# Performance work log

Hardware: AMD Instinct MI355X
Metric: run time of the kernel (lower is better)

Reference implementation:

```python
import jax, jax.numpy as jnp
import numpy as np

B, N, D, HID, NB, NC = 64, 256, 1024, 512, 2, 1000
EPS = 1e-5

def _ln(x, g, b):
    m = x.mean(-1, keepdims=True)
    v = ((x - m) ** 2).mean(-1, keepdims=True)
    return (x - m) / jnp.sqrt(v + EPS) * g + b

def _gelu(x):
    return jax.nn.gelu(x, approximate=False)

def _knn_adjacency(x, k):
    # x: [N, D] -> symmetric-normalized kNN adjacency with self loops, [N, N]
    n = x.shape[0]
    sq = jnp.sum(x * x, axis=-1)
    d2 = sq[:, None] + sq[None, :] - 2.0 * (x @ x.T)
    d2 = jnp.where(jnp.eye(n, dtype=bool), jnp.inf, d2)  # exclude self from kNN
    idx = jax.lax.top_k(-d2, k)[1]                       # [N, k] nearest neighbors
    A = jnp.zeros((n, n), x.dtype).at[jnp.arange(n)[:, None], idx].set(1.0)
    A = jnp.maximum(A, A.T) + jnp.eye(n, dtype=x.dtype)  # symmetrize + self loops
    dinv = jax.lax.rsqrt(A.sum(-1))                      # D^{-1/2}
    return A * dinv[:, None] * dinv[None, :]

def setup_inputs() -> dict:
    key = jax.random.key(0)
    ks = jax.random.split(key, 8)
    s = lambda i, shape: jax.random.normal(ks[i], shape, jnp.float32) * 0.02
    return {
        "tokens": jax.random.normal(ks[0], (B, N, D), jnp.float32),
        "W1": s(1, (NB, D, HID)), "b1": jnp.zeros((NB, HID), jnp.float32),
        "W2": s(2, (NB, HID, D)), "b2": jnp.zeros((NB, D), jnp.float32),
        "g1": jnp.ones((NB, D), jnp.float32), "be1": jnp.zeros((NB, D), jnp.float32),
        "g2": jnp.ones((NB, D), jnp.float32), "be2": jnp.zeros((NB, D), jnp.float32),
        "gr": jnp.ones((D,), jnp.float32), "br": jnp.zeros((D,), jnp.float32),
        "Wc": s(3, (D, NC)), "bc": jnp.zeros((NC,), jnp.float32),
        "k": 8,
    }

def reference(tokens, W1, b1, W2, b2, g1, be1, g2, be2, gr, br, Wc, bc, k):
    # tokens: [B, N, D] backbone features flattened to nodes (eval mode: dropout = identity)
    A = jax.vmap(lambda t: _knn_adjacency(t, k))(tokens)  # [B, N, N]
    x = tokens
    for i in range(NB):  # GraphBlock
        h = _ln(x, g1[i], be1[i])
        h = _gelu(jnp.einsum("bij,bjh->bih", A, h @ W1[i] + b1[i]))  # A_hat @ lin1
        h = jnp.einsum("bij,bjd->bid", A, h @ W2[i] + b2[i])          # A_hat @ lin2
        x = x + h
        x = x + _gelu(_ln(x, g2[i], be2[i]))
    x = _gelu(_ln(x, gr, br))      # readout
    out = x.mean(axis=1)           # graph mean-pool, [B, D]
    return out @ Wc + bc           # logits [B, NC]
```

## Files before the change

### kernel.cpp

```cpp
#include <hip/hip_runtime.h>
#include <hip/hip_bf16.h>
#include <math.h>

constexpr int Bb  = 64;
constexpr int Nn_ = 256;
constexpr int Dd  = 1024;
constexpr int Hh  = 512;
constexpr int NC  = 1000;
constexpr float LN_EPS = 1e-5f;

#define DEV __device__ __forceinline__

typedef unsigned short u16;
typedef __attribute__((ext_vector_type(8))) short bf16x8;
typedef __attribute__((ext_vector_type(4))) float f32x4;
typedef __attribute__((ext_vector_type(4))) unsigned short u16x4;

DEV float erf_fast(float x) {
    const float ax = fabsf(x);
    const float t = __builtin_amdgcn_rcpf(fmaf(0.3275911f, ax, 1.0f));
    const float y = t * (0.254829592f + t * (-0.284496736f + t * (1.421413741f +
                    t * (-1.453152027f + t * 1.061405429f))));
    const float r = 1.0f - y * __expf(-ax * ax);
    return copysignf(r, x);
}
DEV float gelu_f(float x) { return 0.5f * x * (1.0f + erf_fast(x * 0.70710678118654752f)); }
DEV u16 bfb(float x) { __hip_bfloat16 h = __float2bfloat16(x); u16 u; __builtin_memcpy(&u, &h, 2); return u; }
DEV float fromb(u16 u) { unsigned int w = (unsigned int)u << 16; float f; __builtin_memcpy(&f, &w, 4); return f; }

DEV void gload16(const void* g, void* l) {
    __builtin_amdgcn_global_load_lds(
        (const __attribute__((address_space(1))) void*)(uintptr_t)g,
        (__attribute__((address_space(3))) void*)(uintptr_t)l, 16, 0, 0);
}

enum { EP_SBIAS_BF = 3 };

template<int EPI>
__global__ __launch_bounds__(512) void mgemm_k(
    const u16* __restrict__ Ag, const u16* __restrict__ Bg, void* __restrict__ Cg,
    const float* __restrict__ bias, const float* __restrict__ rsA,
    int M, int Nc, int K, long sA, long sB, long sC,
    int lognx, int logny, int lognz)
{
    __shared__ __align__(16) u16 sm[2][2][128 * 32];
    const int tid = threadIdx.x;
    const int l = tid & 63, w = tid >> 6;
    const int wm = w >> 2, wn = w & 3;

    const int lid = blockIdx.x;
    const int xcd = lid & 7, idx = lid >> 3;
    int bxi, byi, z;
    if (lognz == 0) {
        bxi = idx & ((1 << lognx) - 1);
        byi = (xcd << (logny - 3)) | (idx >> lognx);
        z = 0;
    } else {
        bxi = idx & ((1 << lognx) - 1);
        byi = (idx >> lognx) & ((1 << logny) - 1);
        z = (xcd << (lognz - 3)) | (idx >> (lognx + logny));
    }
    const int bm = byi * 128, bn = bxi * 128;

    const u16* Ab  = Ag + (long)z * sA;
    const u16* Bbp = Bg + (long)z * sB;

    f32x4 acc[4][2] = {};
    const int nt = K >> 5;

    auto stage = [&](int db, int t) {
        const long kk = (long)t << 5;
        const int o = tid * 16;
        const int r = o >> 6;
        const int g = ((o >> 4) & 3) ^ ((r >> 1) & 3);
        gload16(Ab  + (long)(bm + r) * K + kk + g * 8, (char*)&sm[db][0][0] + o);
        gload16(Bbp + (long)(bn + r) * K + kk + g * 8, (char*)&sm[db][1][0] + o);
    };

    stage(0, 0);
    __syncthreads();
    for (int t = 0; t < nt; ++t) {
        const int db = t & 1;
        if (t + 1 < nt) stage(db ^ 1, t + 1);
        const int lr = l & 15, g = l >> 4;
        bf16x8 af[4], bfr[2];
        #pragma unroll
        for (int fm = 0; fm < 4; ++fm) {
            const int r = wm * 64 + fm * 16 + lr;
            af[fm] = *(const bf16x8*)((const char*)&sm[db][0][0] + r * 64 + ((g ^ ((r >> 1) & 3)) << 4));
        }
        #pragma unroll
        for (int fn = 0; fn < 2; ++fn) {
            const int r = wn * 32 + fn * 16 + lr;
            bfr[fn] = *(const bf16x8*)((const char*)&sm[db][1][0] + r * 64 + ((g ^ ((r >> 1) & 3)) << 4));
        }
        #pragma unroll
        for (int fm = 0; fm < 4; ++fm)
            #pragma unroll
            for (int fn = 0; fn < 2; ++fn)
                acc[fm][fn] = __builtin_amdgcn_mfma_f32_16x16x32_bf16(af[fm], bfr[fn], acc[fm][fn], 0, 0, 0);
        __syncthreads();
    }

    const int lr = l & 15, lg = l >> 4;
    u16* Cb = (u16*)Cg;
    #pragma unroll
    for (int fm = 0; fm < 4; ++fm)
        #pragma unroll
        for (int fn = 0; fn < 2; ++fn) {
            const int gc = bn + wn * 32 + fn * 16 + lr;
            const float bv = bias[gc];
            #pragma unroll
            for (int rg = 0; rg < 4; ++rg) {
                const int gm = bm + wm * 64 + fm * 16 + lg * 4 + rg;
                Cb[(long)gm * Nc + gc] = bfb(acc[fm][fn][rg] + rsA[gm] * bv);
            }
        }
}

__global__ __launch_bounds__(512) __attribute__((amdgpu_waves_per_eu(2, 2))) void ayy2_k(
    const u16* __restrict__ Ahat, const u16* __restrict__ LN1, const u16* __restrict__ W1t,
    const float* __restrict__ b1, u16* __restrict__ AZ)
{
    __shared__ __align__(16) char smem[131072];
    u16* sY = (u16*)smem;
    u16* sZ = (u16*)(smem + 65536);
    char* stA = smem + 65536;
    char* stB = smem + 65536 + 32768;

    const int tid = threadIdx.x;
    const int l = tid & 63, w = tid >> 6;
    const int lr = l & 15, g = l >> 4;

    const int lid = blockIdx.x;
    const int xcd = lid & 7, idx = lid >> 3;
    const int cs = idx & 3;
    const int z  = xcd * 8 + (idx >> 2);

    const u16* Ab  = Ahat + (long)z * Nn_ * Nn_;
    const u16* Lb  = LN1 + (long)z * Nn_ * Dd;
    const u16* Wsl = W1t + (long)(cs * 128) * Dd;
    const float* bsl = b1 + cs * 128;

    {
        const int rm = w >> 1, cn = w & 1;
        f32x4 acc[4][4] = {};

        auto stage0 = [&](int db, int t) {
            const long kk = (long)t << 5;
            #pragma unroll
            for (int i = 0; i < 2; ++i) {
                const int o = i * 8192 + tid * 16;
                const int r = o >> 6;
                const int gg = ((o >> 4) & 3) ^ ((r >> 1) & 3);
                gload16(Lb + (long)r * Dd + kk + gg * 8, stA + db * 16384 + o);
            }
            {
                const int o = tid * 16;
                const int c = o >> 6;
                const int gg = ((o >> 4) & 3) ^ ((c >> 1) & 3);
                gload16(Wsl + (long)c * Dd + kk + gg * 8, stB + db * 8192 + o);
            }
        };

        stage0(0, 0);
        __syncthreads();
        for (int t = 0; t < 32; ++t) {
            const int db = t & 1;
            if (t + 1 < 32) stage0(db ^ 1, t + 1);
            bf16x8 af[4], bfr[4];
            #pragma unroll
            for (int fm = 0; fm < 4; ++fm) {
                const int r = rm * 64 + fm * 16 + lr;
                af[fm] = *(const bf16x8*)(stA + db * 16384 + r * 64 + ((g ^ ((r >> 1) & 3)) << 4));
            }
            #pragma unroll
            for (int fn = 0; fn < 4; ++fn) {
                const int c = cn * 64 + fn * 16 + lr;
                bfr[fn] = *(const bf16x8*)(stB + db * 8192 + c * 64 + ((g ^ ((c >> 1) & 3)) << 4));
            }
            #pragma unroll
            for (int fm = 0; fm < 4; ++fm)
                #pragma unroll
                for (int fn = 0; fn < 4; ++fn)
                    acc[fm][fn] = __builtin_amdgcn_mfma_f32_16x16x32_bf16(af[fm], bfr[fn], acc[fm][fn], 0, 0, 0);
            __syncthreads();
        }
        #pragma unroll
        for (int fm = 0; fm < 4; ++fm)
            #pragma unroll
            for (int fn = 0; fn < 4; ++fn) {
                const int c = cn * 64 + fn * 16 + lr;
                const int n0 = rm * 64 + fm * 16 + g * 4;
                const float bv = bsl[c];
                u16x4 v;
                #pragma unroll
                for (int rg = 0; rg < 4; ++rg) v[rg] = bfb(acc[fm][fn][rg] + bv);
                *(u16x4*)((char*)sY + c * 512 + ((n0 * 2) ^ ((c & 7) << 4))) = v;
            }
    }

    const int wm = w >> 1, wn = w & 1;
    bf16x8 afh[4][8];
    #pragma unroll
    for (int fm = 0; fm < 4; ++fm) {
        const int r = wm * 64 + fm * 16 + lr;
        #pragma unroll
        for (int ks = 0; ks < 8; ++ks)
            afh[fm][ks] = *(const bf16x8*)(Ab + (long)r * Nn_ + ks * 32 + g * 8);
    }

    __syncthreads();

    f32x4 acc[4][4] = {};
    #pragma unroll
    for (int ks = 0; ks < 8; ++ks) {
        bf16x8 bfr[4];
        #pragma unroll
        for (int fn = 0; fn < 4; ++fn) {
            const int c = wn * 64 + fn * 16 + lr;
            const int kb = (ks * 64 + g * 16) ^ ((c & 7) << 4);
            bfr[fn] = *(const bf16x8*)((const char*)sY + c * 512 + kb);
        }
        #pragma unroll
        for (int fm = 0; fm < 4; ++fm)
            #pragma unroll
            for (int fn = 0; fn < 4; ++fn)
                acc[fm][fn] = __builtin_amdgcn_mfma_f32_16x16x32_bf16(afh[fm][ks], bfr[fn], acc[fm][fn], 0, 0, 0);
    }
    #pragma unroll
    for (int fm = 0; fm < 4; ++fm)
        #pragma unroll
        for (int fn = 0; fn < 4; ++fn) {
            const int c = wn * 64 + fn * 16 + lr;
            const int r0 = wm * 64 + fm * 16 + g * 4;
            u16x4 v;
            #pragma unroll
            for (int rg = 0; rg < 4; ++rg) v[rg] = bfb(gelu_f(acc[fm][fn][rg]));
            *(u16x4*)((char*)sZ + c * 512 + ((r0 * 2) ^ ((c & 7) << 4))) = v;
            acc[fm][fn] = f32x4{0.f, 0.f, 0.f, 0.f};
        }
    __syncthreads();

    #pragma unroll
    for (int ks = 0; ks < 8; ++ks) {
        bf16x8 bfr[4];
        #pragma unroll
        for (int fn = 0; fn < 4; ++fn) {
            const int c = wn * 64 + fn * 16 + lr;
            const int kb = (ks * 64 + g * 16) ^ ((c & 7) << 4);
            bfr[fn] = *(const bf16x8*)((const char*)sZ + c * 512 + kb);
        }
        #pragma unroll
        for (int fm = 0; fm < 4; ++fm)
            #pragma unroll
            for (int fn = 0; fn < 4; ++fn)
                acc[fm][fn] = __builtin_amdgcn_mfma_f32_16x16x32_bf16(afh[fm][ks], bfr[fn], acc[fm][fn], 0, 0, 0);
    }
    u16* Ob = AZ + (long)z * Nn_ * Hh + cs * 128;
    #pragma unroll
    for (int fm = 0; fm < 4; ++fm)
        #pragma unroll
        for (int fn = 0; fn < 4; ++fn)
            #pragma unroll
            for (int rg = 0; rg < 4; ++rg) {
                const int r = wm * 64 + fm * 16 + g * 4 + rg;
                const int c = wn * 64 + fn * 16 + lr;
                Ob[(long)r * Hh + c] = bfb(acc[fm][fn][rg]);
            }
}

__global__ __launch_bounds__(512) void d2mm_k(
    const u16* __restrict__ HL, const float* __restrict__ sq, float* __restrict__ d2)
{
    __shared__ __align__(16) u16 sm[2][4][128 * 32];
    const int tid = threadIdx.x;
    const int l = tid & 63, w = tid >> 6;
    const int wm = w >> 2, wn = w & 3;

    const int lid = blockIdx.x;
    const int xcd = lid & 7, q = lid >> 3;
    const int j   = q % 3;
    const int z   = (q / 3) * 8 + xcd;
    const int bm  = (j == 2) ? 128 : 0;
    const int bn  = (j == 0) ? 0 : 128;

    const u16* Hb = HL + (long)z * Nn_ * 2048;

    f32x4 acc[4][2] = {};

    auto stage = [&](int db, int t) {
        const long kk = (long)t << 5;
        const int o = tid * 16;
        const int r = o >> 6;
        const int g = ((o >> 4) & 3) ^ ((r >> 1) & 3);
        const long ka = kk + g * 8;
        gload16(Hb + (long)(bm + r) * 2048 + ka,        (char*)&sm[db][0][0] + o);
        gload16(Hb + (long)(bm + r) * 2048 + 1024 + ka, (char*)&sm[db][1][0] + o);
        gload16(Hb + (long)(bn + r) * 2048 + ka,        (char*)&sm[db][2][0] + o);
        gload16(Hb + (long)(bn + r) * 2048 + 1024 + ka, (char*)&sm[db][3][0] + o);
    };

    stage(0, 0);
    __syncthreads();
    for (int t = 0; t < 32; ++t) {
        const int db = t & 1;
        if (t + 1 < 32) stage(db ^ 1, t + 1);
        const int lr = l & 15, g = l >> 4;
        bf16x8 ah[4], al[4], bh[2], bl[2];
        #pragma unroll
        for (int fm = 0; fm < 4; ++fm) {
            const int r = wm * 64 + fm * 16 + lr;
            const int off = r * 64 + ((g ^ ((r >> 1) & 3)) << 4);
            ah[fm] = *(const bf16x8*)((const char*)&sm[db][0][0] + off);
            al[fm] = *(const bf16x8*)((const char*)&sm[db][1][0] + off);
        }
        #pragma unroll
        for (int fn = 0; fn < 2; ++fn) {
            const int r = wn * 32 + fn * 16 + lr;
            const int off = r * 64 + ((g ^ ((r >> 1) & 3)) << 4);
            bh[fn] = *(const bf16x8*)((const char*)&sm[db][2][0] + off);
            bl[fn] = *(const bf16x8*)((const char*)&sm[db][3][0] + off);
        }
        #pragma unroll
        for (int fm = 0; fm < 4; ++fm)
            #pragma unroll
            for (int fn = 0; fn < 2; ++fn) {
                acc[fm][fn] = __builtin_amdgcn_mfma_f32_16x16x32_bf16(ah[fm], bh[fn], acc[fm][fn], 0, 0, 0);
                acc[fm][fn] = __builtin_amdgcn_mfma_f32_16x16x32_bf16(ah[fm], bl[fn], acc[fm][fn], 0, 0, 0);
                acc[fm][fn] = __builtin_amdgcn_mfma_f32_16x16x32_bf16(al[fm], bh[fn], acc[fm][fn], 0, 0, 0);
            }
        __syncthreads();
    }

    const int lr = l & 15, lg = l >> 4;
    const float* sqb = sq + z * Nn_;
    float* ob = d2 + (long)z * Nn_ * Nn_;
    #pragma unroll
    for (int fm = 0; fm < 4; ++fm)
        #pragma unroll
        for (int fn = 0; fn < 2; ++fn)
            #pragma unroll
            for (int rg = 0; rg < 4; ++rg) {
                const int gm = bm + wm * 64 + fm * 16 + lg * 4 + rg;
                const int gc = bn + wn * 32 + fn * 16 + lr;
                float v = sqb[gm] + sqb[gc] - 2.0f * acc[fm][fn][rg];
                if (gm == gc) v = INFINITY;
                ob[(long)gm * Nn_ + gc] = v;
                if (j == 1) ob[(long)gc * Nn_ + gm] = v;
            }
}

__global__ __launch_bounds__(256) void clear_k(float4* __restrict__ p)
{
    p[(long)blockIdx.x * 256 + threadIdx.x] = make_float4(0.f, 0.f, 0.f, 0.f);
}

__global__ __launch_bounds__(256) void prep_k(const float* __restrict__ in, u16* __restrict__ hilo,
    float* __restrict__ sq, u16* __restrict__ lnout,
    const float* __restrict__ g, const float* __restrict__ bvec)
{
    const int w = threadIdx.x >> 6, lane = threadIdx.x & 63;
    const long row = (long)blockIdx.x * 4 + w;
    const long base = row * Dd;

    float xs[16];
    #pragma unroll
    for (int c = 0; c < 4; ++c) {
        const int idx = c * 256 + lane * 4;
        const float4 v = *(const float4*)&in[base + idx];
        xs[c*4+0] = v.x; xs[c*4+1] = v.y; xs[c*4+2] = v.z; xs[c*4+3] = v.w;
        u16x4 hi, lo;
        #pragma unroll
        for (int j = 0; j < 4; ++j) {
            hi[j] = bfb(xs[c*4+j]);
            lo[j] = bfb(xs[c*4+j] - fromb(hi[j]));
        }
        *(u16x4*)&hilo[row * 2048 + idx]        = hi;
        *(u16x4*)&hilo[row * 2048 + 1024 + idx] = lo;
    }

    float s = 0.f, s2 = 0.f;
    #pragma unroll
    for (int i = 0; i < 16; ++i) { s += xs[i]; s2 += xs[i] * xs[i]; }
    #pragma unroll
    for (int o = 32; o > 0; o >>= 1) { s += __shfl_xor(s, o); s2 += __shfl_xor(s2, o); }
    if (lane == 0) sq[row] = s2;
    const float mean = s * (1.0f / Dd);
    const float rstd = rsqrtf(s2 * (1.0f / Dd) - mean * mean + LN_EPS);

    #pragma unroll
    for (int c = 0; c < 4; ++c) {
        const int idx = c * 256 + lane * 4;
        const float4 gv = *(const float4*)&g[idx];
        const float4 bv = *(const float4*)&bvec[idx];
        const float gs[4] = {gv.x, gv.y, gv.z, gv.w};
        const float bs[4] = {bv.x, bv.y, bv.z, bv.w};
        u16x4 ov;
        #pragma unroll
        for (int j = 0; j < 4; ++j) ov[j] = bfb((xs[c*4+j] - mean) * rstd * gs[j] + bs[j]);
        *(u16x4*)&lnout[base + idx] = ov;
    }
}

__global__ __launch_bounds__(256) void transw_k(const float* __restrict__ in, u16* __restrict__ out,
                                                int R, int C, long sIn, long sOut)
{
    __shared__ u16 t[32][33];
    const int z = blockIdx.z;
    const float* ib = in + (long)z * sIn;
    u16* ob = out + (long)z * sOut;
    const int r0 = blockIdx.y * 32, c0 = blockIdx.x * 32;
    const int tr = threadIdx.x >> 3, tc4 = (threadIdx.x & 7) * 4;
    const float* p = ib + (long)(r0 + tr) * C + c0 + tc4;
    #pragma unroll
    for (int j = 0; j < 4; ++j) t[tr][tc4 + j] = bfb(p[j]);
    __syncthreads();
    u16* q = ob + (long)(c0 + tr) * R + r0 + tc4;
    #pragma unroll
    for (int j = 0; j < 4; ++j) q[j] = t[tc4 + j][tr];
}

__global__ __launch_bounds__(256) void transc_k(const float* __restrict__ Wc, float* __restrict__ WcT)
{
    __shared__ float t[32][33];
    const int r0 = blockIdx.y * 32, c0 = blockIdx.x * 32;
    const int tr = threadIdx.x >> 3, tc4 = (threadIdx.x & 7) * 4;
    #pragma unroll
    for (int j = 0; j < 4; ++j) {
        const int c = c0 + tc4 + j;
        t[tr][tc4 + j] = (c < NC) ? Wc[(long)(r0 + tr) * NC + c] : 0.f;
    }
    __syncthreads();
    const int oc = c0 + tr;
    if (oc < NC) {
        #pragma unroll
        for (int j = 0; j < 4; ++j)
            WcT[(long)oc * Dd + r0 + tc4 + j] = t[tc4 + j][tr];
    }
}

template<int LAST, int XF32>
__global__ __launch_bounds__(256) void ln2fr_k(const u16* __restrict__ hsrc,
    const void* __restrict__ xinv, u16* __restrict__ xout, u16* __restrict__ lnout,
    const float* __restrict__ g2, const float* __restrict__ be2,
    const float* __restrict__ gn, const float* __restrict__ bn)
{
    const int w = threadIdx.x >> 6, lane = threadIdx.x & 63;
    const long row = (long)blockIdx.x * 4 + w;
    const long base = row * Dd;

    float xs[16];
    #pragma unroll
    for (int c = 0; c < 4; ++c) {
        const int idx = c * 256 + lane * 4;
        const u16x4 hv = *(const u16x4*)&hsrc[base + idx];
        if constexpr (XF32) {
            const float4 xv = *(const float4*)&((const float*)xinv)[base + idx];
            xs[c*4+0] = xv.x + fromb(hv[0]);
            xs[c*4+1] = xv.y + fromb(hv[1]);
            xs[c*4+2] = xv.z + fromb(hv[2]);
            xs[c*4+3] = xv.w + fromb(hv[3]);
        } else {
            const u16x4 xv = *(const u16x4*)&((const u16*)xinv)[base + idx];
            #pragma unroll
            for (int j = 0; j < 4; ++j) xs[c*4+j] = fromb(xv[j]) + fromb(hv[j]);
        }
    }

    {
        float s = 0.f, s2 = 0.f;
        #pragma unroll
        for (int i = 0; i < 16; ++i) { s += xs[i]; s2 += xs[i] * xs[i]; }
        #pragma unroll
        for (int o = 32; o > 0; o >>= 1) { s += __shfl_xor(s, o); s2 += __shfl_xor(s2, o); }
        const float mean = s * (1.0f / Dd);
        const float rstd = rsqrtf(s2 * (1.0f / Dd) - mean * mean + LN_EPS);
        #pragma unroll
        for (int c = 0; c < 4; ++c) {
            const int idx = c * 256 + lane * 4;
            const float4 gv = *(const float4*)&g2[idx];
            const float4 bv = *(const float4*)&be2[idx];
            const float gs[4] = {gv.x, gv.y, gv.z, gv.w};
            const float bs[4] = {bv.x, bv.y, bv.z, bv.w};
            #pragma unroll
            for (int j = 0; j < 4; ++j)
                xs[c*4+j] = xs[c*4+j] + gelu_f((xs[c*4+j] - mean) * rstd * gs[j] + bs[j]);
        }
    }

    float s = 0.f, s2 = 0.f;
    #pragma unroll
    for (int i = 0; i < 16; ++i) { s += xs[i]; s2 += xs[i] * xs[i]; }
    #pragma unroll
    for (int o = 32; o > 0; o >>= 1) { s += __shfl_xor(s, o); s2 += __shfl_xor(s2, o); }
    const float mean = s * (1.0f / Dd);
    const float rstd = rsqrtf(s2 * (1.0f / Dd) - mean * mean + LN_EPS);
    #pragma unroll
    for (int c = 0; c < 4; ++c) {
        const int idx = c * 256 + lane * 4;
        const float4 gv = *(const float4*)&gn[idx];
        const float4 bv = *(const float4*)&bn[idx];
        const float gs[4] = {gv.x, gv.y, gv.z, gv.w};
        const float bs[4] = {bv.x, bv.y, bv.z, bv.w};
        u16x4 ov;
        if constexpr (LAST) {
            #pragma unroll
            for (int j = 0; j < 4; ++j) ov[j] = bfb(gelu_f((xs[c*4+j] - mean) * rstd * gs[j] + bs[j]));
        } else {
            u16x4 xo;
            #pragma unroll
            for (int j = 0; j < 4; ++j) xo[j] = bfb(xs[c*4+j]);
            *(u16x4*)&xout[base + idx] = xo;
            #pragma unroll
            for (int j = 0; j < 4; ++j) ov[j] = bfb((xs[c*4+j] - mean) * rstd * gs[j] + bs[j]);
        }
        *(u16x4*)&lnout[base + idx] = ov;
    }
}

__global__ __launch_bounds__(256) void topk_k(const float* __restrict__ d2, float* __restrict__ Aout,
                                              const int* __restrict__ kptr)
{
    const int k = *kptr;
    const int wid = threadIdx.x >> 6, lane = threadIdx.x & 63;
    const long row = (long)blockIdx.x * 4 + wid;
    const long b = row >> 8;
    const int  i = (int)(row & 255);
    const float* dr = d2 + row * Nn_;
    float v[4];
    bool sel[4] = {false, false, false, false};
    #pragma unroll
    for (int c = 0; c < 4; ++c) v[c] = dr[lane + 64 * c];
    for (int it = 0; it < k; ++it) {
        float bv = INFINITY; int bi = 1 << 20;
        #pragma unroll
        for (int c = 0; c < 4; ++c) {
            const int idx = lane + 64 * c;
            if (!sel[c] && (v[c] < bv || (v[c] == bv && idx < bi))) { bv = v[c]; bi = idx; }
        }
        #pragma unroll
        for (int o = 32; o > 0; o >>= 1) {
            float ov = __shfl_xor(bv, o); int oi = __shfl_xor(bi, o);
            if (ov < bv || (ov == bv && oi < bi)) { bv = ov; bi = oi; }
        }
        #pragma unroll
        for (int c = 0; c < 4; ++c) if (lane + 64 * c == bi) sel[c] = true;
        if (lane == 0) {
            Aout[(b * Nn_ + i) * Nn_ + bi] = 1.0f;
            Aout[(b * Nn_ + bi) * Nn_ + i] = 1.0f;
        }
    }
    if (lane == 0) Aout[(b * Nn_ + i) * Nn_ + i] = 1.0f;
}

__global__ __launch_bounds__(256) void deg_k(const float* __restrict__ A, float* __restrict__ dinv)
{
    const int wid = threadIdx.x >> 6, lane = threadIdx.x & 63;
    const long row = (long)blockIdx.x * 4 + wid;
    const float* ar = A + row * Nn_;
    float s = 0.f;
    #pragma unroll
    for (int c = 0; c < 4; ++c) s += ar[lane + 64 * c];
    #pragma unroll
    for (int o = 32; o > 0; o >>= 1) s += __shfl_down(s, o);
    if (lane == 0) dinv[row] = rsqrtf(s);
}

__global__ __launch_bounds__(256) void scalebf2_k(const float* __restrict__ A, const float* __restrict__ dinv,
                                                  u16* __restrict__ out, float* __restrict__ rsA)
{
    const int wid = threadIdx.x >> 6, lane = threadIdx.x & 63;
    const long row = (long)blockIdx.x * 4 + wid;
    const long b = row >> 8;
    const float di = dinv[row];
    const int j0 = lane * 4;
    const float4 dj = *(const float4*)&dinv[b * Nn_ + j0];
    const float4 a = *(const float4*)&A[row * Nn_ + j0];
    const float v0 = a.x * di * dj.x, v1 = a.y * di * dj.y, v2 = a.z * di * dj.z, v3 = a.w * di * dj.w;
    u16x4 o = { bfb(v0), bfb(v1), bfb(v2), bfb(v3) };
    *(u16x4*)&out[row * Nn_ + j0] = o;
    float s = v0 + v1 + v2 + v3;
    #pragma unroll
    for (int off = 32; off > 0; off >>= 1) s += __shfl_down(s, off);
    if (lane == 0) rsA[row] = s;
}

__global__ __launch_bounds__(256) void poolb_k(const u16* __restrict__ y, float* __restrict__ pooled)
{
    const int d = blockIdx.x * 256 + threadIdx.x;
    const int b = blockIdx.y;
    const u16* yb = y + (long)b * Nn_ * Dd + d;
    float s = 0.f;
    #pragma unroll 4
    for (int n = 0; n < Nn_; ++n) s += fromb(yb[(long)n * Dd]);
    pooled[b * Dd + d] = s * (1.0f / Nn_);
}

__global__ __launch_bounds__(256) void cls2_k(const float* __restrict__ pooled, const float* __restrict__ WcT,
    const float* __restrict__ bc, float* __restrict__ out)
{
    const int w = threadIdx.x >> 6, lane = threadIdx.x & 63;
    const int c = blockIdx.x * 4 + w;
    const int b = blockIdx.y;
    const float* wr = WcT + (long)c * Dd;
    const float* p  = pooled + (long)b * Dd;
    float s = 0.f;
    #pragma unroll
    for (int it = 0; it < 4; ++it) {
        const float4 wv = *(const float4*)&wr[it * 256 + lane * 4];
        const float4 pv = *(const float4*)&p[it * 256 + lane * 4];
        s += wv.x * pv.x + wv.y * pv.y + wv.z * pv.z + wv.w * pv.w;
    }
    #pragma unroll
    for (int o = 32; o > 0; o >>= 1) s += __shfl_down(s, o);
    if (lane == 0) out[(long)b * NC + c] = s + bc[c];
}

extern "C" void kernel_launch(void* const* d_in, const int* in_sizes, int n_in,
                              void* d_out, int out_size, void* d_ws, size_t ws_size,
                              hipStream_t stream)
{
    const float* tokens = (const float*)d_in[0];
    const float* W1  = (const float*)d_in[1];
    const float* b1  = (const float*)d_in[2];
    const float* W2  = (const float*)d_in[3];
    const float* b2  = (const float*)d_in[4];
    const float* g1  = (const float*)d_in[5];
    const float* be1 = (const float*)d_in[6];
    const float* g2  = (const float*)d_in[7];
    const float* be2 = (const float*)d_in[8];
    const float* gr  = (const float*)d_in[9];
    const float* br  = (const float*)d_in[10];
    const float* Wc  = (const float*)d_in[11];
    const float* bc  = (const float*)d_in[12];
    const int*   kptr = (const int*)d_in[13];

    constexpr long SZ_XD = (long)Bb * Nn_ * Dd;
    constexpr long SZ_A  = (long)Bb * Nn_ * Nn_;

    char* wp = (char*)d_ws;
    u16*   xbf    = (u16*)wp;   wp += SZ_XD * 2;
    u16*   hbuf   = (u16*)wp;   wp += SZ_XD * 2;
    u16*   bufA   = (u16*)wp;   wp += SZ_XD * 2;
    u16*   bufB   = (u16*)wp;   wp += SZ_XD * 2;
    u16*   bufC   = (u16*)wp;   wp += SZ_XD * 2;
    u16*   AmatBF = (u16*)wp;   wp += SZ_A * 2;
    u16*   W1t    = (u16*)wp;   wp += 2L * Dd * Hh * 2;
    u16*   W2t    = (u16*)wp;   wp += 2L * Hh * Dd * 2;
    float* WcT    = (float*)wp; wp += (long)NC * Dd * 4;
    float* sq     = (float*)wp; wp += (long)Bb * Nn_ * 4;
    float* dinv   = (float*)wp; wp += (long)Bb * Nn_ * 4;
    float* rsA    = (float*)wp; wp += (long)Bb * Nn_ * 4;
    float* pooled = (float*)wp; wp += (long)Bb * Dd * 4;

    u16*   hilo  = bufA;
    float* d2f   = (float*)hbuf;
    float* AmatF = (float*)xbf;
    u16*   robuf = bufA;

    const dim3 blk(256);
    const dim3 blk8(512);

    prep_k<<<Bb * Nn_ / 4, blk, 0, stream>>>(tokens, hilo, sq, bufC, g1, be1);

    d2mm_k<<<192, blk8, 0, stream>>>(hilo, sq, d2f);
    clear_k<<<(int)(SZ_A / 4 / 256), blk, 0, stream>>>((float4*)AmatF);
    topk_k<<<Bb * Nn_ / 4, blk, 0, stream>>>(d2f, AmatF, kptr);
    deg_k<<<Bb * Nn_ / 4, blk, 0, stream>>>(AmatF, dinv);
    scalebf2_k<<<Bb * Nn_ / 4, blk, 0, stream>>>(AmatF, dinv, AmatBF, rsA);

    transw_k<<<dim3(Hh / 32, Dd / 32, 2), blk, 0, stream>>>(W1, W1t, Dd, Hh, (long)Dd * Hh, (long)Hh * Dd);
    transw_k<<<dim3(Dd / 32, Hh / 32, 2), blk, 0, stream>>>(W2, W2t, Hh, Dd, (long)Hh * Dd, (long)Dd * Hh);
    transc_k<<<dim3(32, Dd / 32), blk, 0, stream>>>(Wc, WcT);

    for (int i = 0; i < 2; ++i) {
        ayy2_k<<<256, blk8, 0, stream>>>(AmatBF, bufC, W1t + (long)i * Hh * Dd, b1 + (long)i * Hh, bufA);
        mgemm_k<EP_SBIAS_BF><<<1024, blk8, 0, stream>>>(
            bufA, W2t + (long)i * Dd * Hh, hbuf, b2 + i * Dd, rsA,
            Bb * Nn_, Dd, Hh, 0, 0, 0, 3, 7, 0);
        if (i == 0)
            ln2fr_k<0, 1><<<Bb * Nn_ / 4, blk, 0, stream>>>(hbuf, tokens, xbf, bufC,
                g2, be2, g1 + Dd, be1 + Dd);
        else
            ln2fr_k<1, 0><<<Bb * Nn_ / 4, blk, 0, stream>>>(hbuf, xbf, nullptr, robuf,
                g2 + Dd, be2 + Dd, gr, br);
    }

    poolb_k<<<dim3(Dd / 256, Bb), blk, 0, stream>>>(robuf, pooled);
    cls2_k<<<dim3(NC / 4, Bb), blk, 0, stream>>>(pooled, WcT, bc, (float*)d_out);
}
```

Measured before the change: 348.5 us.

## Split fused A·(LN·W1) kernel into narrower 64-column slices for more blocks

The fused kernel computing A_hat @ (LN1 @ W1 + b1), GELU, then A_hat @ Z now gives each block 64 hidden columns instead of 128. That doubles the grid to 512 blocks and cuts shared memory from 128KB to 72KB. Each wave now owns 32 rows across all 64 columns rather than a 64x64 tile. The A_hat fragments are re-read from global memory inside each k-step instead of being held in registers, and the waves_per_eu restriction is dropped, which lowers register pressure and raises occupancy. The trade-off is that the LN1 tile is loaded twice as often across blocks, and A_hat is read repeatedly from global memory.

```diff
diff --git a/kernel.cpp b/kernel.cpp
--- a/kernel.cpp
+++ b/kernel.cpp
@@ -118,15 +118,15 @@
         }
 }
 
-__global__ __launch_bounds__(512) __attribute__((amdgpu_waves_per_eu(2, 2))) void ayy2_k(
+__global__ __launch_bounds__(512) void ayy3_k(
     const u16* __restrict__ Ahat, const u16* __restrict__ LN1, const u16* __restrict__ W1t,
     const float* __restrict__ b1, u16* __restrict__ AZ)
 {
-    __shared__ __align__(16) char smem[131072];
-    u16* sY = (u16*)smem;
-    u16* sZ = (u16*)(smem + 65536);
-    char* stA = smem + 65536;
-    char* stB = smem + 65536 + 32768;
+    __shared__ __align__(16) char smem[73728];
+    u16* sY  = (u16*)smem;
+    u16* sZ  = (u16*)(smem + 32768);
+    char* stA = smem + 32768;
+    char* stB = smem + 65536;
 
     const int tid = threadIdx.x;
     const int l = tid & 63, w = tid >> 6;
@@ -134,17 +134,16 @@
 
     const int lid = blockIdx.x;
     const int xcd = lid & 7, idx = lid >> 3;
-    const int cs = idx & 3;
-    const int z  = xcd * 8 + (idx >> 2);
+    const int cs = idx & 7;
+    const int z  = xcd * 8 + (idx >> 3);
 
     const u16* Ab  = Ahat + (long)z * Nn_ * Nn_;
     const u16* Lb  = LN1 + (long)z * Nn_ * Dd;
-    const u16* Wsl = W1t + (long)(cs * 128) * Dd;
-    const float* bsl = b1 + cs * 128;
+    const u16* Wsl = W1t + (long)(cs * 64) * Dd;
+    const float* bsl = b1 + cs * 64;
 
     {
-        const int rm = w >> 1, cn = w & 1;
-        f32x4 acc[4][4] = {};
+        f32x4 acc[2][4] = {};
 
         auto stage0 = [&](int db, int t) {
             const long kk = (long)t << 5;
@@ -155,11 +154,11 @@
                 const int gg = ((o >> 4) & 3) ^ ((r >> 1) & 3);
                 gload16(Lb + (long)r * Dd + kk + gg * 8, stA + db * 16384 + o);
             }
-            {
+            if (w < 4) {
                 const int o = tid * 16;
                 const int c = o >> 6;
                 const int gg = ((o >> 4) & 3) ^ ((c >> 1) & 3);
-                gload16(Wsl + (long)c * Dd + kk + gg * 8, stB + db * 8192 + o);
+                gload16(Wsl + (long)c * Dd + kk + gg * 8, stB + db * 4096 + o);
             }
         };
 
@@ -168,30 +167,30 @@
         for (int t = 0; t < 32; ++t) {
             const int db = t & 1;
             if (t + 1 < 32) stage0(db ^ 1, t + 1);
-            bf16x8 af[4], bfr[4];
-            #pragma unroll
-            for (int fm = 0; fm < 4; ++fm) {
-                const int r = rm * 64 + fm * 16 + lr;
+            bf16x8 af[2], bfr[4];
+            #pragma unroll
+            for (int fm = 0; fm < 2; ++fm) {
+                const int r = w * 32 + fm * 16 + lr;
                 af[fm] = *(const bf16x8*)(stA + db * 16384 + r * 64 + ((g ^ ((r >> 1) & 3)) << 4));
             }
             #pragma unroll
             for (int fn = 0; fn < 4; ++fn) {
-                const int c = cn * 64 + fn * 16 + lr;
-                bfr[fn] = *(const bf16x8*)(stB + db * 8192 + c * 64 + ((g ^ ((c >> 1) & 3)) << 4));
-            }
-            #pragma unroll
-            for (int fm = 0; fm < 4; ++fm)
+                const int c = fn * 16 + lr;
+                bfr[fn] = *(const bf16x8*)(stB + db * 4096 + c * 64 + ((g ^ ((c >> 1) & 3)) << 4));
+            }
+            #pragma unroll
+            for (int fm = 0; fm < 2; ++fm)
                 #pragma unroll
                 for (int fn = 0; fn < 4; ++fn)
                     acc[fm][fn] = __builtin_amdgcn_mfma_f32_16x16x32_bf16(af[fm], bfr[fn], acc[fm][fn], 0, 0, 0);
             __syncthreads();
         }
         #pragma unroll
-        for (int fm = 0; fm < 4; ++fm)
+        for (int fm = 0; fm < 2; ++fm)
             #pragma unroll
             for (int fn = 0; fn < 4; ++fn) {
-                const int c = cn * 64 + fn * 16 + lr;
-                const int n0 = rm * 64 + fm * 16 + g * 4;
+                const int c = fn * 16 + lr;
+                const int n0 = w * 32 + fm * 16 + g * 4;
                 const float bv = bsl[c];
                 u16x4 v;
                 #pragma unroll
@@ -199,41 +198,35 @@
                 *(u16x4*)((char*)sY + c * 512 + ((n0 * 2) ^ ((c & 7) << 4))) = v;
             }
     }
-
-    const int wm = w >> 1, wn = w & 1;
-    bf16x8 afh[4][8];
-    #pragma unroll
-    for (int fm = 0; fm < 4; ++fm) {
-        const int r = wm * 64 + fm * 16 + lr;
-        #pragma unroll
-        for (int ks = 0; ks < 8; ++ks)
-            afh[fm][ks] = *(const bf16x8*)(Ab + (long)r * Nn_ + ks * 32 + g * 8);
-    }
-
     __syncthreads();
 
-    f32x4 acc[4][4] = {};
+    f32x4 acc[2][4] = {};
     #pragma unroll
     for (int ks = 0; ks < 8; ++ks) {
-        bf16x8 bfr[4];
+        bf16x8 af[2], bfr[4];
+        #pragma unroll
+        for (int fm = 0; fm < 2; ++fm) {
+            const int r = w * 32 + fm * 16 + lr;
+            af[fm] = *(const bf16x8*)(Ab + (long)r * Nn_ + ks * 32 + g * 8);
+        }
         #pragma unroll
         for (int fn = 0; fn < 4; ++fn) {
-            const int c = wn * 64 + fn * 16 + lr;
+            const int c = fn * 16 + lr;
             const int kb = (ks * 64 + g * 16) ^ ((c & 7) << 4);
             bfr[fn] = *(const bf16x8*)((const char*)sY + c * 512 + kb);
         }
         #pragma unroll
-        for (int fm = 0; fm < 4; ++fm)
+        for (int fm = 0; fm < 2; ++fm)
             #pragma unroll
             for (int fn = 0; fn < 4; ++fn)
-                acc[fm][fn] = __builtin_amdgcn_mfma_f32_16x16x32_bf16(afh[fm][ks], bfr[fn], acc[fm][fn], 0, 0, 0);
-    }
-    #pragma unroll
-    for (int fm = 0; fm < 4; ++fm)
+                acc[fm][fn] = __builtin_amdgcn_mfma_f32_16x16x32_bf16(af[fm], bfr[fn], acc[fm][fn], 0, 0, 0);
+    }
+    #pragma unroll
+    for (int fm = 0; fm < 2; ++fm)
         #pragma unroll
         for (int fn = 0; fn < 4; ++fn) {
-            const int c = wn * 64 + fn * 16 + lr;
-            const int r0 = wm * 64 + fm * 16 + g * 4;
+            const int c = fn * 16 + lr;
+            const int r0 = w * 32 + fm * 16 + g * 4;
             u16x4 v;
             #pragma unroll
             for (int rg = 0; rg < 4; ++rg) v[rg] = bfb(gelu_f(acc[fm][fn][rg]));
@@ -244,28 +237,33 @@
 
     #pragma unroll
     for (int ks = 0; ks < 8; ++ks) {
-        bf16x8 bfr[4];
+        bf16x8 af[2], bfr[4];
+        #pragma unroll
+        for (int fm = 0; fm < 2; ++fm) {
+            const int r = w * 32 + fm * 16 + lr;
+            af[fm] = *(const bf16x8*)(Ab + (long)r * Nn_ + ks * 32 + g * 8);
+        }
         #pragma unroll
         for (int fn = 0; fn < 4; ++fn) {
-            const int c = wn * 64 + fn * 16 + lr;
+            const int c = fn * 16 + lr;
             const int kb = (ks * 64 + g * 16) ^ ((c & 7) << 4);
             bfr[fn] = *(const bf16x8*)((const char*)sZ + c * 512 + kb);
         }
         #pragma unroll
-        for (int fm = 0; fm < 4; ++fm)
+        for (int fm = 0; fm < 2; ++fm)
             #pragma unroll
             for (int fn = 0; fn < 4; ++fn)
-                acc[fm][fn] = __builtin_amdgcn_mfma_f32_16x16x32_bf16(afh[fm][ks], bfr[fn], acc[fm][fn], 0, 0, 0);
-    }
-    u16* Ob = AZ + (long)z * Nn_ * Hh + cs * 128;
-    #pragma unroll
-    for (int fm = 0; fm < 4; ++fm)
+                acc[fm][fn] = __builtin_amdgcn_mfma_f32_16x16x32_bf16(af[fm], bfr[fn], acc[fm][fn], 0, 0, 0);
+    }
+    u16* Ob = AZ + (long)z * Nn_ * Hh + cs * 64;
+    #pragma unroll
+    for (int fm = 0; fm < 2; ++fm)
         #pragma unroll
         for (int fn = 0; fn < 4; ++fn)
             #pragma unroll
             for (int rg = 0; rg < 4; ++rg) {
-                const int r = wm * 64 + fm * 16 + g * 4 + rg;
-                const int c = wn * 64 + fn * 16 + lr;
+                const int r = w * 32 + fm * 16 + g * 4 + rg;
+                const int c = fn * 16 + lr;
                 Ob[(long)r * Hh + c] = bfb(acc[fm][fn][rg]);
             }
 }
@@ -675,7 +673,7 @@
     transc_k<<<dim3(32, Dd / 32), blk, 0, stream>>>(Wc, WcT);
 
     for (int i = 0; i < 2; ++i) {
-        ayy2_k<<<256, blk8, 0, stream>>>(AmatBF, bufC, W1t + (long)i * Hh * Dd, b1 + (long)i * Hh, bufA);
+        ayy3_k<<<512, blk8, 0, stream>>>(AmatBF, bufC, W1t + (long)i * Hh * Dd, b1 + (long)i * Hh, bufA);
         mgemm_k<EP_SBIAS_BF><<<1024, blk8, 0, stream>>>(
             bufA, W2t + (long)i * Dd * Hh, hbuf, b2 + i * Dd, rsA,
             Bb * Nn_, Dd, Hh, 0, 0, 0, 3, 7, 0);
```

Result: no change. 348.8 us (+0.1%).
